# Optimization experiments

Measured on AMD Instinct MI355X. Metric: run time of the kernel, lower is better.

Reference implementation:

```python
import jax, jax.numpy as jnp
import numpy as np

J = 4                              # wavelet decomposition levels (level[i] = 4 for all experts)
PERM = (0, 1, 2, 3, 4, 5, 4, 5)    # original forward reuses experts 4,5 for gate slots 6,7 (repo bug, kept)


def haar_dwt(x):
    """One level of orthonormal 2D Haar DWT. x: [B,C,H,W] -> (ll [B,C,H/2,W/2], details [B,C,3,H/2,W/2])."""
    x00 = x[..., 0::2, 0::2]
    x01 = x[..., 0::2, 1::2]
    x10 = x[..., 1::2, 0::2]
    x11 = x[..., 1::2, 1::2]
    ll = (x00 + x01 + x10 + x11) * 0.5
    lh = (x00 + x01 - x10 - x11) * 0.5
    hl = (x00 - x01 + x10 - x11) * 0.5
    hh = (x00 - x01 - x10 + x11) * 0.5
    return ll, jnp.stack([lh, hl, hh], axis=2)


def haar_idwt(ll, h):
    """Inverse of haar_dwt. ll: [B,C,m,m], h: [B,C,3,m,m] -> [B,C,2m,2m]."""
    lh, hl, hh = h[:, :, 0], h[:, :, 1], h[:, :, 2]
    x00 = (ll + lh + hl + hh) * 0.5
    x01 = (ll + lh - hl - hh) * 0.5
    x10 = (ll - lh + hl - hh) * 0.5
    x11 = (ll - lh - hl + hh) * 0.5
    B, C, m, _ = ll.shape
    out = jnp.zeros((B, C, 2 * m, 2 * m), ll.dtype)
    out = out.at[..., 0::2, 0::2].set(x00)
    out = out.at[..., 0::2, 1::2].set(x01)
    out = out.at[..., 1::2, 0::2].set(x10)
    out = out.at[..., 1::2, 1::2].set(x11)
    return out


def _expert(x, wl, wh):
    """One WaveConv2d expert: J-level DWT, dense per-mode channel mixing of the coarsest
    approx (wl: [Ci,Co,m,m]) and the 3 coarsest detail bands (wh: [3,Ci,Co,m,m]),
    pass-through of finer detail levels, then inverse DWT."""
    highs = []
    for _ in range(J):
        x, h = haar_dwt(x)
        highs.append(h)
    x = jnp.einsum('bixy,ioxy->boxy', x, wl)
    highs[-1] = jnp.einsum('bikxy,kioxy->bokxy', highs[-1], wh)
    for h in reversed(highs):
        x = haar_idwt(x, h)
    return x


def setup_inputs() -> dict:
    key = jax.random.key(0)
    kx, kl, kw1, kw2 = jax.random.split(key, 4)
    B, C, S = 32, 64, 64
    m = S >> J                       # coarsest-level mode count = 4
    scale = 1.0 / (C * C)
    x = jax.random.normal(kx, (B, C, S, S), jnp.float32)
    lambda_ = jax.random.uniform(kl, (B, 1, 8, 1), dtype=jnp.float32)
    WL = scale * jax.random.uniform(kw1, (8, C, C, m, m), dtype=jnp.float32)
    WH = scale * jax.random.uniform(kw2, (8, 3, C, C, m, m), dtype=jnp.float32)
    return {"x": x, "lambda_": lambda_, "WL": WL, "WH": WH}


def reference(x, lambda_, WL, WH):
    # Only experts 0..5 are ever called by the original forward (6,7 are dead params).
    ys = jax.vmap(_expert, in_axes=(None, 0, 0))(x, WL[:6], WH[:6])   # [6,B,C,H,W]
    ys = ys[jnp.asarray(PERM)]                                        # [8,B,C,H,W]
    gate = jnp.moveaxis(lambda_, 2, 0)[..., None]                     # [8,B,1,1,1]
    return jnp.sum(gate * ys, axis=0)                                 # [B,C,H,W]
```

## Files before the change

### kernel.cpp

```cpp
#include <hip/hip_runtime.h>


#define COEF_N 131072

typedef float floatx4 __attribute__((ext_vector_type(4)));

__global__ __launch_bounds__(256) void kA(const float* __restrict__ x,
                                          const float* __restrict__ WL,
                                          const float* __restrict__ WH,
                                          float* __restrict__ coef,
                                          float* __restrict__ wpack2) {
  int bi = blockIdx.x;
  int tid = threadIdx.x;
  if (bi < 512) {
    int b = bi >> 4;
    int cg = bi & 15;
    int wave = tid >> 6;
    int lane = tid & 63;
    int c = cg * 4 + wave;
    const float4* img4 = (const float4*)(x + (size_t)(b * 64 + c) * 4096);
    int col4 = lane & 15;
    int rgrp = lane >> 4;
    float top[4] = {0.f, 0.f, 0.f, 0.f}, bot[4] = {0.f, 0.f, 0.f, 0.f};
#pragma unroll
    for (int t = 0; t < 16; ++t) {
      int row = t * 4 + rgrp;
      float4 v = img4[row * 16 + col4];
      float s = v.x + v.y + v.z + v.w;
      if ((t & 3) < 2) top[t >> 2] += s;
      else             bot[t >> 2] += s;
    }
    float sc = ((col4 & 3) < 2) ? 1.0f : -1.0f;
    int Y = col4 >> 2;
#pragma unroll
    for (int X = 0; X < 4; ++X) {
      float s = top[X] + bot[X];
      float d = top[X] - bot[X];
      float r[4];
      r[0] = s; r[1] = d; r[2] = sc * s; r[3] = sc * d;
#pragma unroll
      for (int band = 0; band < 4; ++band) {
        float v = r[band];
        v += __shfl_xor(v, 1, 64);
        v += __shfl_xor(v, 2, 64);
        v += __shfl_xor(v, 16, 64);
        v += __shfl_xor(v, 32, 64);
        if ((lane & 3) == 0 && rgrp == 0) {
          coef[(((band * 4 + X) * 4 + Y) * 32 + b) * 64 + c] = v * 0.0625f;
        }
      }
    }
  } else {
    int gid = (bi - 512) * 256 + tid;
    int o = gid & 63;
    int i = (gid >> 6) & 63;
    int be = gid >> 12;
    int e = be % 6;
    int band = be / 6;
    const float* src;
    if (band == 0) src = WL + (size_t)((e * 64 + i) * 64 + o) * 16;
    else           src = WH + (size_t)(((e * 3 + (band - 1)) * 64 + i) * 64 + o) * 16;
    const float4* s4 = (const float4*)src;
    float4 v0 = s4[0], v1 = s4[1], v2 = s4[2], v3 = s4[3];
    float vv[16] = {v0.x, v0.y, v0.z, v0.w, v1.x, v1.y, v1.z, v1.w,
                    v2.x, v2.y, v2.z, v2.w, v3.x, v3.y, v3.z, v3.w};
    int ei = e * 64 + i;
    int eg = ei >> 2, er = ei & 3;
#pragma unroll
    for (int xy = 0; xy < 16; ++xy) {
      int bxy = band * 16 + xy;
      wpack2[(((size_t)bxy * 96 + eg) * 64 + o) * 4 + er] = vv[xy];
    }
  }
}

__global__ __launch_bounds__(512) void kB(const float* __restrict__ coef,
                                          const float* __restrict__ wpack2,
                                          const float* __restrict__ lam,
                                          float* __restrict__ delta) {
  __shared__ float4 Agv[384][8];
  __shared__ float rawA[32][65];
  __shared__ float gg[32][8];
  int bxy = blockIdx.x;
  int tid = threadIdx.x;
  const float* cslab = coef + (size_t)bxy * 2048;
  for (int idx = tid; idx < 2048; idx += 512) rawA[idx >> 6][idx & 63] = cslab[idx];
  if (tid < 32) {
    int b = tid;
    float l[8];
#pragma unroll
    for (int j = 0; j < 8; ++j) l[j] = lam[b * 8 + j];
    gg[b][0] = l[0]; gg[b][1] = l[1]; gg[b][2] = l[2]; gg[b][3] = l[3];
    gg[b][4] = l[4] + l[6];
    gg[b][5] = l[5] + l[7];
    gg[b][6] = l[0] + l[1] + l[2] + l[3] + l[4] + l[5] + l[6] + l[7];
  }
  __syncthreads();
  for (int idx = tid; idx < 384 * 8; idx += 512) {
    int ei = idx >> 3, bq = idx & 7;
    int e = ei >> 6, i = ei & 63;
    float4 a;
    a.x = gg[bq * 4 + 0][e] * rawA[bq * 4 + 0][i];
    a.y = gg[bq * 4 + 1][e] * rawA[bq * 4 + 1][i];
    a.z = gg[bq * 4 + 2][e] * rawA[bq * 4 + 2][i];
    a.w = gg[bq * 4 + 3][e] * rawA[bq * 4 + 3][i];
    Agv[ei][bq] = a;
  }
  __syncthreads();
  int o = tid & 63;
  int bq = tid >> 6;
  const float4* wp = (const float4*)wpack2 + (size_t)bxy * (96 * 64) + o;
  float acc0 = 0.f, acc1 = 0.f, acc2 = 0.f, acc3 = 0.f;
  for (int eg = 0; eg < 96; ++eg) {
    float4 w = wp[(size_t)eg * 64];
    float4 a0 = Agv[eg * 4 + 0][bq];
    float4 a1 = Agv[eg * 4 + 1][bq];
    float4 a2 = Agv[eg * 4 + 2][bq];
    float4 a3 = Agv[eg * 4 + 3][bq];
    acc0 += a0.x * w.x + a1.x * w.y + a2.x * w.z + a3.x * w.w;
    acc1 += a0.y * w.x + a1.y * w.y + a2.y * w.z + a3.y * w.w;
    acc2 += a0.z * w.x + a1.z * w.y + a2.z * w.z + a3.z * w.w;
    acc3 += a0.w * w.x + a1.w * w.y + a2.w * w.z + a3.w * w.w;
  }
  float* dslab = delta + (size_t)bxy * 2048;
  float G0 = gg[bq * 4 + 0][6], G1 = gg[bq * 4 + 1][6];
  float G2 = gg[bq * 4 + 2][6], G3 = gg[bq * 4 + 3][6];
  dslab[(bq * 4 + 0) * 64 + o] = acc0 - G0 * rawA[bq * 4 + 0][o];
  dslab[(bq * 4 + 1) * 64 + o] = acc1 - G1 * rawA[bq * 4 + 1][o];
  dslab[(bq * 4 + 2) * 64 + o] = acc2 - G2 * rawA[bq * 4 + 2][o];
  dslab[(bq * 4 + 3) * 64 + o] = acc3 - G3 * rawA[bq * 4 + 3][o];
}

__global__ __launch_bounds__(256) void kC(const float* __restrict__ x,
                                          const float* __restrict__ delta,
                                          const float* __restrict__ lam,
                                          float* __restrict__ out) {
  int bo = blockIdx.x;
  int b = bo >> 6, o = bo & 63;
  int tid = threadIdx.x;
  __shared__ float ds[64];
  if (tid < 64) {
    int band = tid >> 4, xy = tid & 15;
    ds[tid] = delta[((size_t)(band * 16 + xy) * 32 + b) * 64 + o];
  }
  __syncthreads();
  float G = 0.f;
#pragma unroll
  for (int j = 0; j < 8; ++j) G += lam[b * 8 + j];
  int w4 = tid & 15;
  int h0 = tid >> 4;
  int Y = w4 >> 2;
  float sc = ((w4 & 3) < 2) ? 1.f : -1.f;
  float sr = (h0 < 8) ? 1.f : -1.f;
  const float4* xi = (const float4*)(x + (size_t)bo * 4096);
  floatx4* oi = (floatx4*)(out + (size_t)bo * 4096);
#pragma unroll
  for (int X = 0; X < 4; ++X) {
    float dsel = (ds[X * 4 + Y] + sr * ds[16 + X * 4 + Y] +
                  sc * ds[32 + X * 4 + Y] + sr * sc * ds[48 + X * 4 + Y]) * 0.0625f;
    int idx = (X * 16 + h0) * 16 + w4;
    float4 v = xi[idx];
    floatx4 r;
    r.x = G * v.x + dsel;
    r.y = G * v.y + dsel;
    r.z = G * v.z + dsel;
    r.w = G * v.w + dsel;
    __builtin_nontemporal_store(r, &oi[idx]);
  }
}

extern "C" void kernel_launch(void* const* d_in, const int* in_sizes, int n_in,
                              void* d_out, int out_size, void* d_ws, size_t ws_size,
                              hipStream_t stream) {
  const float* x   = (const float*)d_in[0];
  const float* lam = (const float*)d_in[1];
  const float* WL  = (const float*)d_in[2];
  const float* WH  = (const float*)d_in[3];
  float* out = (float*)d_out;
  float* coef   = (float*)d_ws;
  float* delta  = coef + COEF_N;
  float* wpack2 = delta + COEF_N;

  hipLaunchKernelGGL(kA, dim3(896), dim3(256), 0, stream, x, WL, WH, coef, wpack2);
  hipLaunchKernelGGL(kB, dim3(64), dim3(512), 0, stream, coef, wpack2, lam, delta);
  hipLaunchKernelGGL(kC, dim3(2048), dim3(256), 0, stream, x, delta, lam, out);
}
```

Measured before the change: 113.7 us.

## Split kB reduction over expert-channel dimension into four partial blocks

The kB contraction over 384 expert-input channels is split into four quarter-slices, one per block, raising the grid from 64 to 256 blocks so more compute units on the GPU are busy. Each block writes a partial delta slab, and kC sums the four partials when loading its coefficients. This trades a larger delta workspace and four scattered loads per coefficient in kC for better parallelism in the small GEMM-like stage.

```diff
diff --git a/kernel.cpp b/kernel.cpp
--- a/kernel.cpp
+++ b/kernel.cpp
@@ -2,6 +2,7 @@
 
 
 #define COEF_N 131072
+#define DELTA_N (4 * COEF_N)
 
 typedef float floatx4 __attribute__((ext_vector_type(4)));
 
@@ -78,10 +79,12 @@
                                           const float* __restrict__ wpack2,
                                           const float* __restrict__ lam,
                                           float* __restrict__ delta) {
-  __shared__ float4 Agv[384][8];
+  __shared__ float4 Agv[96][8];
   __shared__ float rawA[32][65];
   __shared__ float gg[32][8];
-  int bxy = blockIdx.x;
+  int blk = blockIdx.x;
+  int bxy = blk >> 2;
+  int q = blk & 3;
   int tid = threadIdx.x;
   const float* cslab = coef + (size_t)bxy * 2048;
   for (int idx = tid; idx < 2048; idx += 512) rawA[idx >> 6][idx & 63] = cslab[idx];
@@ -96,22 +99,24 @@
     gg[b][6] = l[0] + l[1] + l[2] + l[3] + l[4] + l[5] + l[6] + l[7];
   }
   __syncthreads();
-  for (int idx = tid; idx < 384 * 8; idx += 512) {
-    int ei = idx >> 3, bq = idx & 7;
+  for (int idx = tid; idx < 96 * 8; idx += 512) {
+    int eil = idx >> 3, bq = idx & 7;
+    int ei = q * 96 + eil;
     int e = ei >> 6, i = ei & 63;
     float4 a;
     a.x = gg[bq * 4 + 0][e] * rawA[bq * 4 + 0][i];
     a.y = gg[bq * 4 + 1][e] * rawA[bq * 4 + 1][i];
     a.z = gg[bq * 4 + 2][e] * rawA[bq * 4 + 2][i];
     a.w = gg[bq * 4 + 3][e] * rawA[bq * 4 + 3][i];
-    Agv[ei][bq] = a;
+    Agv[eil][bq] = a;
   }
   __syncthreads();
   int o = tid & 63;
   int bq = tid >> 6;
-  const float4* wp = (const float4*)wpack2 + (size_t)bxy * (96 * 64) + o;
+  const float4* wp = (const float4*)wpack2 + (size_t)bxy * (96 * 64) +
+                     (size_t)(q * 24) * 64 + o;
   float acc0 = 0.f, acc1 = 0.f, acc2 = 0.f, acc3 = 0.f;
-  for (int eg = 0; eg < 96; ++eg) {
+  for (int eg = 0; eg < 24; ++eg) {
     float4 w = wp[(size_t)eg * 64];
     float4 a0 = Agv[eg * 4 + 0][bq];
     float4 a1 = Agv[eg * 4 + 1][bq];
@@ -122,13 +127,20 @@
     acc2 += a0.z * w.x + a1.z * w.y + a2.z * w.z + a3.z * w.w;
     acc3 += a0.w * w.x + a1.w * w.y + a2.w * w.z + a3.w * w.w;
   }
-  float* dslab = delta + (size_t)bxy * 2048;
-  float G0 = gg[bq * 4 + 0][6], G1 = gg[bq * 4 + 1][6];
-  float G2 = gg[bq * 4 + 2][6], G3 = gg[bq * 4 + 3][6];
-  dslab[(bq * 4 + 0) * 64 + o] = acc0 - G0 * rawA[bq * 4 + 0][o];
-  dslab[(bq * 4 + 1) * 64 + o] = acc1 - G1 * rawA[bq * 4 + 1][o];
-  dslab[(bq * 4 + 2) * 64 + o] = acc2 - G2 * rawA[bq * 4 + 2][o];
-  dslab[(bq * 4 + 3) * 64 + o] = acc3 - G3 * rawA[bq * 4 + 3][o];
+  float* dslab = delta + (size_t)(q * 64 + bxy) * 2048;
+  if (q == 0) {
+    float G0 = gg[bq * 4 + 0][6], G1 = gg[bq * 4 + 1][6];
+    float G2 = gg[bq * 4 + 2][6], G3 = gg[bq * 4 + 3][6];
+    dslab[(bq * 4 + 0) * 64 + o] = acc0 - G0 * rawA[bq * 4 + 0][o];
+    dslab[(bq * 4 + 1) * 64 + o] = acc1 - G1 * rawA[bq * 4 + 1][o];
+    dslab[(bq * 4 + 2) * 64 + o] = acc2 - G2 * rawA[bq * 4 + 2][o];
+    dslab[(bq * 4 + 3) * 64 + o] = acc3 - G3 * rawA[bq * 4 + 3][o];
+  } else {
+    dslab[(bq * 4 + 0) * 64 + o] = acc0;
+    dslab[(bq * 4 + 1) * 64 + o] = acc1;
+    dslab[(bq * 4 + 2) * 64 + o] = acc2;
+    dslab[(bq * 4 + 3) * 64 + o] = acc3;
+  }
 }
 
 __global__ __launch_bounds__(256) void kC(const float* __restrict__ x,
@@ -141,7 +153,12 @@
   __shared__ float ds[64];
   if (tid < 64) {
     int band = tid >> 4, xy = tid & 15;
-    ds[tid] = delta[((size_t)(band * 16 + xy) * 32 + b) * 64 + o];
+    float s = 0.f;
+#pragma unroll
+    for (int q = 0; q < 4; ++q) {
+      s += delta[((size_t)(q * 64 + band * 16 + xy) * 32 + b) * 64 + o];
+    }
+    ds[tid] = s;
   }
   __syncthreads();
   float G = 0.f;
@@ -179,9 +196,9 @@
   float* out = (float*)d_out;
   float* coef   = (float*)d_ws;
   float* delta  = coef + COEF_N;
-  float* wpack2 = delta + COEF_N;
+  float* wpack2 = delta + DELTA_N;
 
   hipLaunchKernelGGL(kA, dim3(896), dim3(256), 0, stream, x, WL, WH, coef, wpack2);
-  hipLaunchKernelGGL(kB, dim3(64), dim3(512), 0, stream, coef, wpack2, lam, delta);
+  hipLaunchKernelGGL(kB, dim3(256), dim3(512), 0, stream, coef, wpack2, lam, delta);
   hipLaunchKernelGGL(kC, dim3(2048), dim3(256), 0, stream, x, delta, lam, out);
 }
```

Measured after the change: 107.9 us. 5.1% less time.
